# Performance work log

Hardware: AMD Instinct MI355X
Metric: run time of the kernel (lower is better)

The kernel has to match this reference:

```python
import jax, jax.numpy as jnp
import numpy as np

NUM_NODES = 100000
NUM_EDGES = 1_600_000
FEAT = 32


def setup_inputs() -> dict:
    key = jax.random.key(0)
    k1, k2 = jax.random.split(key)
    msg = jax.random.normal(k1, (NUM_EDGES, FEAT), dtype=jnp.float32)
    edge_index = jax.random.randint(k2, (2, NUM_EDGES), 0, NUM_NODES, dtype=jnp.int64)
    return {"msg": msg, "edge_index": edge_index, "num_nodes": NUM_NODES}


def reference(msg, edge_index, num_nodes):
    # Scatter-add edge messages into target nodes (edge_index[1]).
    target_nodes = edge_index[1]
    # segment_sum == zeros(num_nodes, feat).at[target].add(msg)
    out = jax.ops.segment_sum(msg, target_nodes, num_segments=num_nodes)
    return out
```

## Files before the change

### kernel.cpp

```cpp
#include <hip/hip_runtime.h>


#define FEAT    32
#define NPB     128
#define CHUNK   16384
#define SCAN_BS 1024
#define PART_BS 256
#define MAXB    1024
#define RU      16

__global__ void bucket_hist_kernel(const int* __restrict__ tgt, int* __restrict__ hist,
                                   int E, int nblk, int NB) {
    __shared__ int h[MAXB];
    for (int k = threadIdx.x; k < NB; k += blockDim.x) h[k] = 0;
    __syncthreads();
    int base = blockIdx.x * CHUNK;
    int end = min(base + CHUNK, E);
    for (int i = base + threadIdx.x; i < end; i += blockDim.x)
        atomicAdd(&h[tgt[i] >> 7], 1);
    __syncthreads();
    for (int k = threadIdx.x; k < NB; k += blockDim.x)
        hist[k * nblk + blockIdx.x] = h[k];
}

__global__ void scan_block_kernel(const int* __restrict__ in, int* __restrict__ off,
                                  int* __restrict__ psum, int M) {
    __shared__ int s[SCAN_BS];
    int i = blockIdx.x * SCAN_BS + threadIdx.x;
    s[threadIdx.x] = (i < M) ? in[i] : 0;
    __syncthreads();
    for (int d = 1; d < SCAN_BS; d <<= 1) {
        int t = (threadIdx.x >= d) ? s[threadIdx.x - d] : 0;
        __syncthreads();
        s[threadIdx.x] += t;
        __syncthreads();
    }
    if (i < M) off[i + 1] = s[threadIdx.x];
    if (threadIdx.x == SCAN_BS - 1) psum[blockIdx.x] = s[SCAN_BS - 1];
}

__global__ void scan_partials_kernel(int* __restrict__ psum, int nb) {
    __shared__ int s[PART_BS];
    int run = 0;
    for (int base = 0; base < nb; base += PART_BS) {
        int i = base + threadIdx.x;
        int v = (i < nb) ? psum[i] : 0;
        s[threadIdx.x] = v;
        __syncthreads();
        for (int d = 1; d < PART_BS; d <<= 1) {
            int t = (threadIdx.x >= d) ? s[threadIdx.x - d] : 0;
            __syncthreads();
            s[threadIdx.x] += t;
            __syncthreads();
        }
        if (i < nb) psum[i] = run + s[threadIdx.x] - v;
        run += s[PART_BS - 1];
        __syncthreads();
    }
}

__global__ void finalize_offsets_kernel(int* __restrict__ off, const int* __restrict__ psum,
                                        int M) {
    int i = blockIdx.x * SCAN_BS + threadIdx.x;
    if (i == 0) off[0] = 0;
    if (i < M) off[i + 1] += psum[blockIdx.x];
}

__global__ void scatter_pack_kernel(const int* __restrict__ tgt, const int* __restrict__ off,
                                    int* __restrict__ packed, int E, int nblk, int NB) {
    __shared__ int cur[MAXB];
    for (int k = threadIdx.x; k < NB; k += blockDim.x)
        cur[k] = off[k * nblk + blockIdx.x];
    __syncthreads();
    int base = blockIdx.x * CHUNK;
    int end = min(base + CHUNK, E);
    for (int i = base + threadIdx.x; i < end; i += blockDim.x) {
        int t = tgt[i];
        int pos = atomicAdd(&cur[t >> 7], 1);
        packed[pos] = ((t & (NPB - 1)) << 24) | i;
    }
}

__global__ __launch_bounds__(512, 6)
void bucket_reduce_kernel(const float* __restrict__ msg,
                          const int* __restrict__ packed,
                          const int* __restrict__ off,
                          float* __restrict__ out,
                          int E, int nblk, int NB, int N) {
    __shared__ float acc[NPB * FEAT];
    for (int i = threadIdx.x; i < NPB * FEAT; i += blockDim.x) acc[i] = 0.f;
    __syncthreads();
    int k = blockIdx.x;
    int s0 = off[k * nblk];
    int s1 = (k + 1 < NB) ? off[(k + 1) * nblk] : E;
    int slot = threadIdx.x >> 5;
    int f = threadIdx.x & 31;
    for (int j = s0; j < s1; j += 16 * RU) {
        int p[RU];
        float m[RU];
#pragma unroll
        for (int u = 0; u < RU; ++u) {
            int jj = j + u * 16 + slot;
            p[u] = packed[jj < s1 ? jj : s1 - 1];
        }
#pragma unroll
        for (int u = 0; u < RU; ++u)
            m[u] = msg[(size_t)(p[u] & 0xFFFFFF) * FEAT + f];
#pragma unroll
        for (int u = 0; u < RU; ++u) {
            int jj = j + u * 16 + slot;
            if (jj < s1)
                atomicAdd(&acc[(p[u] >> 24) * FEAT + f], m[u]);
        }
    }
    __syncthreads();
    int nodebase = k * NPB;
    for (int i = threadIdx.x; i < NPB * FEAT; i += blockDim.x) {
        int l = i >> 5;
        if (nodebase + l < N)
            out[(size_t)(nodebase + l) * FEAT + (i & 31)] = acc[i];
    }
}

extern "C" void kernel_launch(void* const* d_in, const int* in_sizes, int n_in,
                              void* d_out, int out_size, void* d_ws, size_t ws_size,
                              hipStream_t stream) {
    const float* msg = (const float*)d_in[0];
    const int* edge_index = (const int*)d_in[1];
    int E = in_sizes[0] / FEAT;
    int N = out_size / FEAT;
    const int* tgt = edge_index + E;

    int NB   = (N + NPB - 1) / NPB;
    int nblk = (E + CHUNK - 1) / CHUNK;
    int M    = NB * nblk;
    int nb2  = (M + SCAN_BS - 1) / SCAN_BS;

    int* hist   = (int*)d_ws;
    int* off    = hist + M;
    int* psum   = off + M + 1;
    int* packed = psum + nb2;

    bucket_hist_kernel<<<nblk, 512, 0, stream>>>(tgt, hist, E, nblk, NB);
    scan_block_kernel<<<nb2, SCAN_BS, 0, stream>>>(hist, off, psum, M);
    scan_partials_kernel<<<1, PART_BS, 0, stream>>>(psum, nb2);
    finalize_offsets_kernel<<<nb2, SCAN_BS, 0, stream>>>(off, psum, M);
    scatter_pack_kernel<<<nblk, 512, 0, stream>>>(tgt, off, packed, E, nblk, NB);
    bucket_reduce_kernel<<<NB, 512, 0, stream>>>(msg, packed, off, (float*)d_out,
                                                 E, nblk, NB, N);
}
```

Before: 595.2 us.

## Halve bucket size, use 32-bit offset inline-asm loads, add atomic fallback

Reduces nodes per bucket from 128 to 64 and doubles the histogram chunk, which halves the shared accumulator so more blocks fit per CU (launch bounds raised to 8). In the reduce kernel, message loads become hand-written global_load_dword instructions using 32-bit byte offsets from an SGPR base, followed by an explicit wait and a scheduling barrier to force all loads in flight before the LDS atomics. It also adds a plain global-atomic scatter path for when the workspace is too small. Risks: the 32-bit offset overflows for larger edge counts, the bucket end now reads off[NB*nblk], which relies on the last scan offset equalling E, and the forced full wait may serialise load and atomic phases.

```diff
diff --git a/kernel.cpp b/kernel.cpp
--- a/kernel.cpp
+++ b/kernel.cpp
@@ -2,12 +2,13 @@
 
 
 #define FEAT    32
-#define NPB     128
-#define CHUNK   16384
+#define NPB     64
+#define CHUNK   32768
 #define SCAN_BS 1024
 #define PART_BS 256
-#define MAXB    1024
+#define MAXB    2048
 #define RU      16
+#define NSLOT   16
 
 __global__ void bucket_hist_kernel(const int* __restrict__ tgt, int* __restrict__ hist,
                                    int E, int nblk, int NB) {
@@ -17,7 +18,7 @@
     int base = blockIdx.x * CHUNK;
     int end = min(base + CHUNK, E);
     for (int i = base + threadIdx.x; i < end; i += blockDim.x)
-        atomicAdd(&h[tgt[i] >> 7], 1);
+        atomicAdd(&h[tgt[i] >> 6], 1);
     __syncthreads();
     for (int k = threadIdx.x; k < NB; k += blockDim.x)
         hist[k * nblk + blockIdx.x] = h[k];
@@ -76,12 +77,12 @@
     int end = min(base + CHUNK, E);
     for (int i = base + threadIdx.x; i < end; i += blockDim.x) {
         int t = tgt[i];
-        int pos = atomicAdd(&cur[t >> 7], 1);
+        int pos = atomicAdd(&cur[t >> 6], 1);
         packed[pos] = ((t & (NPB - 1)) << 24) | i;
     }
 }
 
-__global__ __launch_bounds__(512, 6)
+__global__ __launch_bounds__(512, 8)
 void bucket_reduce_kernel(const float* __restrict__ msg,
                           const int* __restrict__ packed,
                           const int* __restrict__ off,
@@ -92,23 +93,30 @@
     __syncthreads();
     int k = blockIdx.x;
     int s0 = off[k * nblk];
-    int s1 = (k + 1 < NB) ? off[(k + 1) * nblk] : E;
+    int s1 = off[(k + 1) * nblk];
     int slot = threadIdx.x >> 5;
     int f = threadIdx.x & 31;
-    for (int j = s0; j < s1; j += 16 * RU) {
+    for (int j = s0; j < s1; j += NSLOT * RU) {
         int p[RU];
+        int o32[RU];
         float m[RU];
 #pragma unroll
         for (int u = 0; u < RU; ++u) {
-            int jj = j + u * 16 + slot;
+            int jj = j + u * NSLOT + slot;
             p[u] = packed[jj < s1 ? jj : s1 - 1];
         }
 #pragma unroll
         for (int u = 0; u < RU; ++u)
-            m[u] = msg[(size_t)(p[u] & 0xFFFFFF) * FEAT + f];
+            o32[u] = ((p[u] & 0xFFFFFF) << 7) + (f << 2);
+#pragma unroll
+        for (int u = 0; u < RU; ++u)
+            asm volatile("global_load_dword %0, %1, %2"
+                         : "=v"(m[u]) : "v"(o32[u]), "s"(msg) : "memory");
+        asm volatile("s_waitcnt vmcnt(0)" ::: "memory");
+        __builtin_amdgcn_sched_barrier(0);
 #pragma unroll
         for (int u = 0; u < RU; ++u) {
-            int jj = j + u * 16 + slot;
+            int jj = j + u * NSLOT + slot;
             if (jj < s1)
                 atomicAdd(&acc[(p[u] >> 24) * FEAT + f], m[u]);
         }
@@ -120,6 +128,19 @@
         if (nodebase + l < N)
             out[(size_t)(nodebase + l) * FEAT + (i & 31)] = acc[i];
     }
+}
+
+__global__ void scatter_add_kernel(const float4* __restrict__ msg4,
+                                   const int* __restrict__ tgt,
+                                   float* __restrict__ out, int num_edges) {
+    int i = blockIdx.x * blockDim.x + threadIdx.x;
+    if (i >= num_edges * (FEAT / 4)) return;
+    int e = i >> 3, q = i & 7;
+    float4 mm = msg4[i];
+    int t = tgt[e];
+    float* dst = out + (size_t)t * FEAT + q * 4;
+    atomicAdd(dst + 0, mm.x); atomicAdd(dst + 1, mm.y);
+    atomicAdd(dst + 2, mm.z); atomicAdd(dst + 3, mm.w);
 }
 
 extern "C" void kernel_launch(void* const* d_in, const int* in_sizes, int n_in,
@@ -136,6 +157,14 @@
     int M    = NB * nblk;
     int nb2  = (M + SCAN_BS - 1) / SCAN_BS;
 
+    size_t need = ((size_t)M + (M + 1) + nb2 + E) * sizeof(int);
+    if (ws_size < need) {
+        hipMemsetAsync(d_out, 0, (size_t)out_size * sizeof(float), stream);
+        int total = E * (FEAT / 4);
+        scatter_add_kernel<<<(total + 255) / 256, 256, 0, stream>>>(
+            (const float4*)msg, tgt, (float*)d_out, E);
+        return;
+    }
     int* hist   = (int*)d_ws;
     int* off    = hist + M;
     int* psum   = off + M + 1;
```

Measured after the change: 574.7 us. 1.04x faster.
